# Kernel tuning notes

Measured on AMD Instinct MI355X. Metric: run time of the kernel, lower is better.

## Reference

```python
import jax, jax.numpy as jnp
import numpy as np

EMBED_DIM = 1024
NUM_HEADS = 16
HEAD_DIM = EMBED_DIM // NUM_HEADS


def setup_inputs() -> dict:
    key = jax.random.key(0)
    k1, k2, k3, k4 = jax.random.split(key, 4)
    B, S, D = 2, 2048, EMBED_DIM
    x = jax.random.normal(k1, (B, S, D), dtype=jnp.float32)
    xpos = jax.random.randint(k2, (B, S), 0, 2048, dtype=jnp.int32)
    # torch nn.Linear weights: [out_features, in_features]; qkv_bias=False -> no qkv bias
    qkv_w = jax.random.normal(k3, (3 * D, D), dtype=jnp.float32) * (D ** -0.5)
    proj_w = jax.random.normal(k4, (D, D), dtype=jnp.float32) * (D ** -0.5)
    proj_b = jnp.zeros((D,), dtype=jnp.float32)
    return {"x": x, "xpos": xpos, "qkv_w": qkv_w, "proj_w": proj_w, "proj_b": proj_b}


def reference(x, xpos, qkv_w, proj_w, proj_b):
    # rope is None, dropout rates are 0, so xpos is unused and dropout is identity.
    B, S, D = x.shape
    H, hd = NUM_HEADS, D // NUM_HEADS
    scale = hd ** -0.5

    qkv = x @ qkv_w.T                                   # [B, S, 3D]
    qkv = qkv.reshape(B, S, 3, H, hd)
    qkv = jnp.transpose(qkv, (0, 3, 2, 1, 4))           # [B, H, 3, S, hd]
    q, k, v = qkv[:, :, 0], qkv[:, :, 1], qkv[:, :, 2]  # each [B, H, S, hd]

    scores = jnp.einsum("bhqd,bhkd->bhqk", q, k) * scale  # [B, H, S, S]
    probs = jax.nn.softmax(scores, axis=-1)
    out = jnp.einsum("bhqk,bhkd->bhqd", probs, v)         # [B, H, S, hd]

    out = jnp.transpose(out, (0, 2, 1, 3)).reshape(B, S, D)
    out = out @ proj_w.T + proj_b
    return out
```

## Files before the change

kernel.cpp:

```cpp
#include <hip/hip_runtime.h>


typedef __bf16 bf16_8 __attribute__((ext_vector_type(8)));
typedef __bf16 bf16_4 __attribute__((ext_vector_type(4)));
typedef __bf16 bf16_2 __attribute__((ext_vector_type(2)));
typedef float floatx4 __attribute__((ext_vector_type(4)));

#define MFMA16 __builtin_amdgcn_mfma_f32_16x16x32_bf16
#define CSCALE 0.1803368801111204f
#define EXP2R  __builtin_amdgcn_exp2f

__device__ __forceinline__ void gld16(const __bf16* g, __bf16* l) {
    __builtin_amdgcn_global_load_lds(
        (const __attribute__((address_space(1))) void*)g,
        (__attribute__((address_space(3))) void*)l, 16, 0, 0);
}

__device__ __forceinline__ unsigned pk_bf16(float a, float b) {
    bf16_2 t;
    t[0] = (__bf16)a; t[1] = (__bf16)b;
    return __builtin_bit_cast(unsigned, t);
}

__global__ __launch_bounds__(256) void cvt_all(
    const float* __restrict__ x, const float* __restrict__ w1,
    const float* __restrict__ w2,
    __bf16* __restrict__ xb, __bf16* __restrict__ w1b, __bf16* __restrict__ w2b)
{
    const int i = blockIdx.x * 256 + threadIdx.x;
    const float* src; __bf16* dst; int off;
    if (i < (1 << 20))                  { src = x;  dst = xb;  off = i; }
    else if (i < (1 << 20) + 786432)    { src = w1; dst = w1b; off = i - (1 << 20); }
    else                                { src = w2; dst = w2b; off = i - (1 << 20) - 786432; }
    float4 v = ((const float4*)src)[off];
    bf16_4 o;
    o[0] = (__bf16)v.x; o[1] = (__bf16)v.y; o[2] = (__bf16)v.z; o[3] = (__bf16)v.w;
    ((bf16_4*)dst)[off] = o;
}

__global__ __launch_bounds__(512) void qkv_gemm(
    const __bf16* __restrict__ X, const __bf16* __restrict__ W,
    __bf16* __restrict__ q_ws, __bf16* __restrict__ k_ws, __bf16* __restrict__ vt_ws)
{
    __shared__ __align__(16) __bf16 S[2][2][128 * 64];

    const int tid = threadIdx.x, lane = tid & 63;
    const int half = tid >> 8, htid = tid & 255;
    const int wvh = (tid >> 6) & 3;
    const int quad = lane >> 4, l15 = lane & 15;
    const int wm = (wvh >> 1) * 64, wn = (wvh & 1) * 64;
    const int m0 = blockIdx.y * 128, n0 = blockIdx.x * 128;
    const int c = n0 >> 10;

    const __bf16* Abase;
    const __bf16* Bbase;
    if (c == 2) { Abase = X + (size_t)m0 * 1024; Bbase = W + (size_t)n0 * 1024; }
    else        { Abase = W + (size_t)n0 * 1024; Bbase = X + (size_t)m0 * 1024; }
    Abase += half * 512;
    Bbase += half * 512;

    __bf16* As = S[half][0];
    __bf16* Bs = S[half][1];
    floatx4 acc[4][4] = {};

    for (int k0 = 0; k0 < 512; k0 += 64) {
        __syncthreads();
#pragma unroll
        for (int it = 0; it < 4; ++it) {
            int cc = it * 256 + htid;
            int row = cc >> 3, kc = cc & 7;
            gld16(Abase + row * 1024 + k0 + ((kc ^ (row & 7)) * 8), &As[cc * 8]);
        }
#pragma unroll
        for (int it = 0; it < 4; ++it) {
            int cc = it * 256 + htid;
            int row = cc >> 3, kc = cc & 7;
            gld16(Bbase + row * 1024 + k0 + ((kc ^ (row & 7)) * 8), &Bs[cc * 8]);
        }
        __syncthreads();

#pragma unroll
        for (int ks = 0; ks < 2; ++ks) {
            bf16_8 af[4], bf[4];
#pragma unroll
            for (int mt = 0; mt < 4; ++mt) {
                int r = wm + mt * 16 + l15;
                af[mt] = *(const bf16_8*)&As[r * 64 + (((ks * 4 + quad) ^ (r & 7)) * 8)];
            }
#pragma unroll
            for (int nt = 0; nt < 4; ++nt) {
                int r = wn + nt * 16 + l15;
                bf[nt] = *(const bf16_8*)&Bs[r * 64 + (((ks * 4 + quad) ^ (r & 7)) * 8)];
            }
#pragma unroll
            for (int mt = 0; mt < 4; ++mt)
#pragma unroll
                for (int nt = 0; nt < 4; ++nt)
                    acc[mt][nt] = MFMA16(af[mt], bf[nt], acc[mt][nt], 0, 0, 0);
        }
    }

    __syncthreads();
    float* comb = (float*)S;
    if (half == 1) {
#pragma unroll
        for (int mt = 0; mt < 4; ++mt)
#pragma unroll
            for (int nt = 0; nt < 4; ++nt)
                *(floatx4*)&comb[((mt * 4 + nt) * 256 + htid) * 4] = acc[mt][nt];
    }
    __syncthreads();
    if (half != 0) return;

#pragma unroll
    for (int mt = 0; mt < 4; ++mt)
#pragma unroll
        for (int nt = 0; nt < 4; ++nt)
            acc[mt][nt] += *(const floatx4*)&comb[((mt * 4 + nt) * 256 + htid) * 4];

    if (c == 2) {
#pragma unroll
        for (int mt = 0; mt < 4; ++mt) {
            const int mbase = m0 + wm + mt * 16 + quad * 4;
            const int b = mbase >> 11, s = mbase & 2047;
#pragma unroll
            for (int nt = 0; nt < 4; ++nt) {
                const int n = n0 + wn + nt * 16 + l15;
                const int h = (n >> 6) & 15, d = n & 63;
                bf16_4 pk;
#pragma unroll
                for (int r = 0; r < 4; ++r) pk[r] = (__bf16)acc[mt][nt][r];
                *(bf16_4*)&vt_ws[((b * 16 + h) * 64 + d) * 2048 + s] = pk;
            }
        }
    } else {
        __bf16* dst = (c == 0) ? q_ws : k_ws;
        const float scale = (c == 1) ? CSCALE : 1.0f;
#pragma unroll
        for (int mt = 0; mt < 4; ++mt) {
            const int nn = n0 + wm + mt * 16 + quad * 4;
            const int h = (nn >> 6) & 15, d0 = nn & 63;
#pragma unroll
            for (int nt = 0; nt < 4; ++nt) {
                const int token = m0 + wn + nt * 16 + l15;
                const int b = token >> 11, s = token & 2047;
                bf16_4 pk;
#pragma unroll
                for (int r = 0; r < 4; ++r) pk[r] = (__bf16)(acc[mt][nt][r] * scale);
                *(bf16_4*)&dst[((b * 16 + h) * 2048 + s) * 64 + d0] = pk;
            }
        }
    }
}

__global__ __launch_bounds__(512) void attn_kernel(
    const __bf16* __restrict__ q_ws, const __bf16* __restrict__ k_ws,
    const __bf16* __restrict__ vt_ws, __bf16* __restrict__ attn_ws)
{
    __shared__ __align__(16) __bf16 Ks [2][64 * 64];
    __shared__ __align__(16) __bf16 Vts[2][64 * 64];
    __shared__ __align__(16) __bf16 Ps [8][16][72];

    const int tid = threadIdx.x, lane = tid & 63, w = tid >> 6;
    const int quad = lane >> 4, l15 = lane & 15;
    const int bh = blockIdx.x, qt = blockIdx.y;
    const int q0 = qt * 128;

    const __bf16* qp  = q_ws  + (size_t)bh * (2048 * 64);
    const __bf16* kp  = k_ws  + (size_t)bh * (2048 * 64);
    const __bf16* vtp = vt_ws + (size_t)bh * (64 * 2048);

    const int srow = tid >> 3, skc = tid & 7;
    const int sw   = (skc ^ (srow & 7)) * 8;
    const __bf16* kb = kp  + (size_t)srow * 64 + sw;
    const __bf16* vb = vtp + (size_t)srow * 2048 + sw;
    const int ldsoff = tid * 8;

    bf16_8 qf[2];
    {
        const int qrow = q0 + w * 16 + l15;
        qf[0] = *(const bf16_8*)&qp[qrow * 64 + quad * 8];
        qf[1] = *(const bf16_8*)&qp[qrow * 64 + 32 + quad * 8];
    }

    bf16_8 ones;
#pragma unroll
    for (int j = 0; j < 8; ++j) ones[j] = (__bf16)1.0f;

    floatx4 oacc[4] = {};
    floatx4 lsum = {};

    gld16(kb, &Ks[0][ldsoff]);
    gld16(vb, &Vts[0][ldsoff]);
    __syncthreads();

#pragma unroll 2
    for (int kt = 0; kt < 32; ++kt) {
        const int cur = kt & 1;
        if (kt < 31) {
            gld16(kb + (size_t)(kt + 1) * 4096, &Ks[cur ^ 1][ldsoff]);
            gld16(vb + (size_t)(kt + 1) * 64,   &Vts[cur ^ 1][ldsoff]);
        }
        const __bf16* Kb = Ks[cur];
        const __bf16* Vb = Vts[cur];

        floatx4 sacc[4] = {};
        __builtin_amdgcn_s_setprio(1);
#pragma unroll
        for (int ks = 0; ks < 2; ++ks)
#pragma unroll
            for (int kg = 0; kg < 4; ++kg) {
                const int krow = kg * 16 + l15;
                bf16_8 kf = *(const bf16_8*)&Kb[krow * 64 + (((ks * 4 + quad) ^ (krow & 7)) * 8)];
                sacc[kg] = MFMA16(kf, qf[ks], sacc[kg], 0, 0, 0);
            }
        __builtin_amdgcn_s_setprio(0);

#pragma unroll
        for (int kg = 0; kg < 4; ++kg) {
            uint2 pk;
            pk.x = pk_bf16(EXP2R(sacc[kg][0]), EXP2R(sacc[kg][1]));
            pk.y = pk_bf16(EXP2R(sacc[kg][2]), EXP2R(sacc[kg][3]));
            *(uint2*)&Ps[w][l15][kg * 16 + quad * 4] = pk;
        }
        __asm__ __volatile__("s_waitcnt lgkmcnt(0)" ::: "memory");

        __builtin_amdgcn_s_setprio(1);
#pragma unroll
        for (int ks = 0; ks < 2; ++ks) {
            bf16_8 pf = *(const bf16_8*)&Ps[w][l15][ks * 32 + quad * 8];
            lsum = MFMA16(ones, pf, lsum, 0, 0, 0);
#pragma unroll
            for (int dg = 0; dg < 4; ++dg) {
                const int drow = dg * 16 + l15;
                bf16_8 vf = *(const bf16_8*)&Vb[drow * 64 + (((ks * 4 + quad) ^ (drow & 7)) * 8)];
                oacc[dg] = MFMA16(vf, pf, oacc[dg], 0, 0, 0);
            }
        }
        __builtin_amdgcn_s_setprio(0);

        if (kt < 31) {
            __asm__ __volatile__("s_waitcnt vmcnt(0)" ::: "memory");
            __syncthreads();
        }
    }

    const int b = bh >> 4, h = bh & 15;
    const float inv_l = 1.0f / lsum[0];
    const int token = b * 2048 + q0 + w * 16 + l15;
#pragma unroll
    for (int dg = 0; dg < 4; ++dg) {
        bf16_4 ok;
#pragma unroll
        for (int r = 0; r < 4; ++r) ok[r] = (__bf16)(oacc[dg][r] * inv_l);
        *(bf16_4*)&attn_ws[(size_t)token * 1024 + h * 64 + dg * 16 + quad * 4] = ok;
    }
}

__device__ __forceinline__ void proj_stage(
    const __bf16* __restrict__ A, const __bf16* __restrict__ Bp,
    int k0, __bf16* As, __bf16* Bs, int tid)
{
#pragma unroll
    for (int it = 0; it < 4; ++it) {
        int cc = it * 256 + tid;
        int row = cc >> 3, kc = cc & 7;
        gld16(A + row * 1024 + k0 + ((kc ^ (row & 7)) * 8), &As[cc * 8]);
    }
#pragma unroll
    for (int it = 0; it < 2; ++it) {
        int cc = it * 256 + tid;
        int row = cc >> 3, kc = cc & 7;
        gld16(Bp + row * 1024 + k0 + ((kc ^ (row & 7)) * 8), &Bs[cc * 8]);
    }
}

__global__ __launch_bounds__(256) void proj_gemm(
    const __bf16* __restrict__ Ain, const __bf16* __restrict__ W,
    const float* __restrict__ bias, float* __restrict__ out)
{
    __shared__ __align__(16) __bf16 As[2][128 * 64];
    __shared__ __align__(16) __bf16 Bs[2][64 * 64];
    floatx4 acc[4][2] = {};
    const int m0 = blockIdx.y * 128, n0 = blockIdx.x * 64;

    const int tid = threadIdx.x, lane = tid & 63, wv = tid >> 6;
    const int quad = lane >> 4, l15 = lane & 15;
    const int wm = (wv >> 1) * 64, wn = (wv & 1) * 32;

    const __bf16* A  = Ain + (size_t)m0 * 1024;
    const __bf16* Bp = W   + (size_t)n0 * 1024;

    proj_stage(A, Bp, 0, As[0], Bs[0], tid);
    __syncthreads();

#pragma unroll 2
    for (int kk = 0; kk < 16; ++kk) {
        const int cur = kk & 1;
        if (kk < 15)
            proj_stage(A, Bp, (kk + 1) * 64, As[cur ^ 1], Bs[cur ^ 1], tid);

        const __bf16* Ab = As[cur];
        const __bf16* Bb = Bs[cur];
#pragma unroll
        for (int ks = 0; ks < 2; ++ks) {
            bf16_8 af[4], bf[2];
#pragma unroll
            for (int mt = 0; mt < 4; ++mt) {
                int r = wm + mt * 16 + l15;
                af[mt] = *(const bf16_8*)&Ab[r * 64 + (((ks * 4 + quad) ^ (r & 7)) * 8)];
            }
#pragma unroll
            for (int nt = 0; nt < 2; ++nt) {
                int r = wn + nt * 16 + l15;
                bf[nt] = *(const bf16_8*)&Bb[r * 64 + (((ks * 4 + quad) ^ (r & 7)) * 8)];
            }
#pragma unroll
            for (int mt = 0; mt < 4; ++mt)
#pragma unroll
                for (int nt = 0; nt < 2; ++nt)
                    acc[mt][nt] = MFMA16(af[mt], bf[nt], acc[mt][nt], 0, 0, 0);
        }

        if (kk < 15) {
            __asm__ __volatile__("s_waitcnt vmcnt(0)" ::: "memory");
            __syncthreads();
        }
    }

    float bv[2];
#pragma unroll
    for (int nt = 0; nt < 2; ++nt) bv[nt] = bias[n0 + wn + nt * 16 + l15];

#pragma unroll
    for (int mt = 0; mt < 4; ++mt) {
        const int m = m0 + wm + mt * 16 + quad * 4;
#pragma unroll
        for (int nt = 0; nt < 2; ++nt) {
            const int n = n0 + wn + nt * 16 + l15;
#pragma unroll
            for (int r = 0; r < 4; ++r)
                out[(size_t)(m + r) * 1024 + n] = acc[mt][nt][r] + bv[nt];
        }
    }
}

extern "C" void kernel_launch(void* const* d_in, const int* in_sizes, int n_in,
                              void* d_out, int out_size, void* d_ws, size_t ws_size,
                              hipStream_t stream)
{
    const float* x      = (const float*)d_in[0];
    const float* qkv_w  = (const float*)d_in[2];
    const float* proj_w = (const float*)d_in[3];
    const float* proj_b = (const float*)d_in[4];
    float* out = (float*)d_out;

    const size_t SZ   = 4096 * 1024;
    const size_t WQKV = 3072 * 1024;
    const size_t WPRJ = 1024 * 1024;

    __bf16* xb      = (__bf16*)d_ws;
    __bf16* qkvwb   = xb + SZ;
    __bf16* projwb  = qkvwb + WQKV;
    __bf16* q_ws    = projwb + WPRJ;
    __bf16* k_ws    = q_ws + SZ;
    __bf16* vt_ws   = k_ws + SZ;
    __bf16* attn_ws = vt_ws + SZ;

    cvt_all<<<dim3(8192), 256, 0, stream>>>(x, qkv_w, proj_w, xb, qkvwb, projwb);
    qkv_gemm  <<<dim3(24, 32), 512, 0, stream>>>(xb, qkvwb, q_ws, k_ws, vt_ws);
    attn_kernel<<<dim3(32, 16), 512, 0, stream>>>(q_ws, k_ws, vt_ws, attn_ws);
    proj_gemm <<<dim3(16, 32), 256, 0, stream>>>(attn_ws, projwb, proj_b, out);
}
```

Before: 183.9 us.

## Switch attention to 32x32 MFMA with register-resident P via permlane swap

The attention kernel now uses 32x32x16 bf16 MFMA tiles, with each wave owning 32 query rows, and the block shrinks to 256 threads. The P tile is no longer staged through LDS. Exponentiated scores are packed in registers and rearranged with v_permlane32_swap into the B-operand layout for the PV MFMA. The row sum is now accumulated in scalar VALU adds plus one cross-half shuffle, replacing the ones-vector MFMA. This removes LDS writes and reads and a wait per tile, in exchange for more registers per lane and half as many threads loading each K/V tile.

Result: slower. 188.6 us (+2.6%).

```diff
diff --git a/kernel.cpp b/kernel.cpp
--- a/kernel.cpp
+++ b/kernel.cpp
@@ -5,8 +5,11 @@
 typedef __bf16 bf16_4 __attribute__((ext_vector_type(4)));
 typedef __bf16 bf16_2 __attribute__((ext_vector_type(2)));
 typedef float floatx4 __attribute__((ext_vector_type(4)));
+typedef float floatx16 __attribute__((ext_vector_type(16)));
+typedef unsigned uintx4 __attribute__((ext_vector_type(4)));
 
 #define MFMA16 __builtin_amdgcn_mfma_f32_16x16x32_bf16
+#define MFMA32 __builtin_amdgcn_mfma_f32_32x32x16_bf16
 #define CSCALE 0.1803368801111204f
 #define EXP2R  __builtin_amdgcn_exp2f
 
@@ -20,6 +23,10 @@
     bf16_2 t;
     t[0] = (__bf16)a; t[1] = (__bf16)b;
     return __builtin_bit_cast(unsigned, t);
+}
+
+__device__ __forceinline__ void pl32swap(unsigned& a, unsigned& b) {
+    __asm__ __volatile__("v_permlane32_swap_b32 %0, %1" : "+v"(a), "+v"(b));
 }
 
 __global__ __launch_bounds__(256) void cvt_all(
@@ -153,16 +160,15 @@
     }
 }
 
-__global__ __launch_bounds__(512) void attn_kernel(
+__global__ __launch_bounds__(256) void attn_kernel(
     const __bf16* __restrict__ q_ws, const __bf16* __restrict__ k_ws,
     const __bf16* __restrict__ vt_ws, __bf16* __restrict__ attn_ws)
 {
     __shared__ __align__(16) __bf16 Ks [2][64 * 64];
     __shared__ __align__(16) __bf16 Vts[2][64 * 64];
-    __shared__ __align__(16) __bf16 Ps [8][16][72];
 
     const int tid = threadIdx.x, lane = tid & 63, w = tid >> 6;
-    const int quad = lane >> 4, l15 = lane & 15;
+    const int l31 = lane & 31, hi = lane >> 5;
     const int bh = blockIdx.x, qt = blockIdx.y;
     const int q0 = qt * 128;
 
@@ -176,65 +182,80 @@
     const __bf16* vb = vtp + (size_t)srow * 2048 + sw;
     const int ldsoff = tid * 8;
 
-    bf16_8 qf[2];
+    bf16_8 qf[4];
     {
-        const int qrow = q0 + w * 16 + l15;
-        qf[0] = *(const bf16_8*)&qp[qrow * 64 + quad * 8];
-        qf[1] = *(const bf16_8*)&qp[qrow * 64 + 32 + quad * 8];
-    }
-
-    bf16_8 ones;
-#pragma unroll
-    for (int j = 0; j < 8; ++j) ones[j] = (__bf16)1.0f;
-
-    floatx4 oacc[4] = {};
-    floatx4 lsum = {};
-
-    gld16(kb, &Ks[0][ldsoff]);
-    gld16(vb, &Vts[0][ldsoff]);
+        const int qrow = q0 + w * 32 + l31;
+#pragma unroll
+        for (int s = 0; s < 4; ++s)
+            qf[s] = *(const bf16_8*)&qp[qrow * 64 + s * 16 + hi * 8];
+    }
+
+    floatx16 oacc[2] = {};
+    float lsum = 0.f;
+
+    gld16(kb,             &Ks [0][ldsoff]);
+    gld16(kb + 32 * 64,   &Ks [0][ldsoff + 2048]);
+    gld16(vb,             &Vts[0][ldsoff]);
+    gld16(vb + 32 * 2048, &Vts[0][ldsoff + 2048]);
     __syncthreads();
 
 #pragma unroll 2
     for (int kt = 0; kt < 32; ++kt) {
         const int cur = kt & 1;
         if (kt < 31) {
-            gld16(kb + (size_t)(kt + 1) * 4096, &Ks[cur ^ 1][ldsoff]);
-            gld16(vb + (size_t)(kt + 1) * 64,   &Vts[cur ^ 1][ldsoff]);
+            const __bf16* kn = kb + (size_t)(kt + 1) * 4096;
+            const __bf16* vn = vb + (size_t)(kt + 1) * 64;
+            gld16(kn,             &Ks [cur ^ 1][ldsoff]);
+            gld16(kn + 32 * 64,   &Ks [cur ^ 1][ldsoff + 2048]);
+            gld16(vn,             &Vts[cur ^ 1][ldsoff]);
+            gld16(vn + 32 * 2048, &Vts[cur ^ 1][ldsoff + 2048]);
         }
         const __bf16* Kb = Ks[cur];
         const __bf16* Vb = Vts[cur];
 
-        floatx4 sacc[4] = {};
+        floatx16 sacc[2] = {};
         __builtin_amdgcn_s_setprio(1);
 #pragma unroll
-        for (int ks = 0; ks < 2; ++ks)
-#pragma unroll
-            for (int kg = 0; kg < 4; ++kg) {
-                const int krow = kg * 16 + l15;
-                bf16_8 kf = *(const bf16_8*)&Kb[krow * 64 + (((ks * 4 + quad) ^ (krow & 7)) * 8)];
-                sacc[kg] = MFMA16(kf, qf[ks], sacc[kg], 0, 0, 0);
-            }
+        for (int s = 0; s < 4; ++s) {
+            const int kc = s * 2 + hi;
+#pragma unroll
+            for (int t = 0; t < 2; ++t) {
+                const int row = t * 32 + l31;
+                bf16_8 kf = *(const bf16_8*)&Kb[row * 64 + ((kc ^ (row & 7)) * 8)];
+                sacc[t] = MFMA32(kf, qf[s], sacc[t], 0, 0, 0);
+            }
+        }
         __builtin_amdgcn_s_setprio(0);
 
-#pragma unroll
-        for (int kg = 0; kg < 4; ++kg) {
-            uint2 pk;
-            pk.x = pk_bf16(EXP2R(sacc[kg][0]), EXP2R(sacc[kg][1]));
-            pk.y = pk_bf16(EXP2R(sacc[kg][2]), EXP2R(sacc[kg][3]));
-            *(uint2*)&Ps[w][l15][kg * 16 + quad * 4] = pk;
-        }
-        __asm__ __volatile__("s_waitcnt lgkmcnt(0)" ::: "memory");
+        unsigned D[2][4][2];
+#pragma unroll
+        for (int t = 0; t < 2; ++t)
+#pragma unroll
+            for (int j = 0; j < 4; ++j)
+#pragma unroll
+                for (int e = 0; e < 2; ++e) {
+                    float pa = EXP2R(sacc[t][j * 4 + e * 2]);
+                    float pb = EXP2R(sacc[t][j * 4 + e * 2 + 1]);
+                    lsum += pa + pb;
+                    D[t][j][e] = pk_bf16(pa, pb);
+                }
 
         __builtin_amdgcn_s_setprio(1);
 #pragma unroll
-        for (int ks = 0; ks < 2; ++ks) {
-            bf16_8 pf = *(const bf16_8*)&Ps[w][l15][ks * 32 + quad * 8];
-            lsum = MFMA16(ones, pf, lsum, 0, 0, 0);
-#pragma unroll
-            for (int dg = 0; dg < 4; ++dg) {
-                const int drow = dg * 16 + l15;
-                bf16_8 vf = *(const bf16_8*)&Vb[drow * 64 + (((ks * 4 + quad) ^ (drow & 7)) * 8)];
-                oacc[dg] = MFMA16(vf, pf, oacc[dg], 0, 0, 0);
+        for (int s = 0; s < 4; ++s) {
+            const int t = s >> 1, b2 = (s & 1) * 2;
+            unsigned x0 = D[t][b2][0], y0 = D[t][b2 + 1][0];
+            unsigned x1 = D[t][b2][1], y1 = D[t][b2 + 1][1];
+            pl32swap(x0, y0);
+            pl32swap(x1, y1);
+            uintx4 u; u[0] = x0; u[1] = x1; u[2] = y0; u[3] = y1;
+            const bf16_8 pf = __builtin_bit_cast(bf16_8, u);
+            const int kc = s * 2 + hi;
+#pragma unroll
+            for (int dt = 0; dt < 2; ++dt) {
+                const int row = dt * 32 + l31;
+                bf16_8 vf = *(const bf16_8*)&Vb[row * 64 + ((kc ^ (row & 7)) * 8)];
+                oacc[dt] = MFMA32(vf, pf, oacc[dt], 0, 0, 0);
             }
         }
         __builtin_amdgcn_s_setprio(0);
@@ -246,15 +267,19 @@
     }
 
     const int b = bh >> 4, h = bh & 15;
-    const float inv_l = 1.0f / lsum[0];
-    const int token = b * 2048 + q0 + w * 16 + l15;
-#pragma unroll
-    for (int dg = 0; dg < 4; ++dg) {
-        bf16_4 ok;
-#pragma unroll
-        for (int r = 0; r < 4; ++r) ok[r] = (__bf16)(oacc[dg][r] * inv_l);
-        *(bf16_4*)&attn_ws[(size_t)token * 1024 + h * 64 + dg * 16 + quad * 4] = ok;
-    }
+    const float lpart = __shfl_xor(lsum, 32, 64);
+    const float inv_l = 1.0f / (lsum + lpart);
+    const int token = b * 2048 + q0 + w * 32 + l31;
+#pragma unroll
+    for (int dt = 0; dt < 2; ++dt)
+#pragma unroll
+        for (int g = 0; g < 4; ++g) {
+            bf16_4 ok;
+#pragma unroll
+            for (int r = 0; r < 4; ++r)
+                ok[r] = (__bf16)(oacc[dt][g * 4 + r] * inv_l);
+            *(bf16_4*)&attn_ws[(size_t)token * 1024 + h * 64 + dt * 32 + g * 8 + hi * 4] = ok;
+        }
 }
 
 __device__ __forceinline__ void proj_stage(
@@ -369,6 +394,6 @@
 
     cvt_all<<<dim3(8192), 256, 0, stream>>>(x, qkv_w, proj_w, xb, qkvwb, projwb);
     qkv_gemm  <<<dim3(24, 32), 512, 0, stream>>>(xb, qkvwb, q_ws, k_ws, vt_ws);
-    attn_kernel<<<dim3(32, 16), 512, 0, stream>>>(q_ws, k_ws, vt_ws, attn_ws);
+    attn_kernel<<<dim3(32, 16), 256, 0, stream>>>(q_ws, k_ws, vt_ws, attn_ws);
     proj_gemm <<<dim3(16, 32), 256, 0, stream>>>(attn_ws, projwb, proj_b, out);
 }
```
